# Kernel optimization log

Measured on AMD Instinct MI355X. Metric: run time of the kernel, lower is better.

Reference implementation:

```python
import jax, jax.numpy as jnp
import numpy as np

N, C, H = 4096, 1024, 16
HD = C // H            # 64
DR = HD // 8           # 8 rope freqs per spatial axis


def setup_inputs() -> dict:
    key = jax.random.key(0)
    k1, k2, k3, k4, k5, k6 = jax.random.split(key, 6)
    x = jax.random.normal(k1, (N, C), dtype=jnp.float32)
    coords = jax.random.randint(k2, (N, 5), 0, 64, dtype=jnp.int32)  # [batch, t, h, w, z]
    w_qkv = jax.random.normal(k3, (3 * C, C), dtype=jnp.float32) / np.sqrt(C)
    w_out = jax.random.normal(k4, (C, C), dtype=jnp.float32) / np.sqrt(C)
    gamma_q = jnp.ones((H, HD), dtype=jnp.float32)
    gamma_k = jnp.ones((H, HD), dtype=jnp.float32)
    return {"x": x, "coords": coords, "w_qkv": w_qkv, "w_out": w_out,
            "gamma_q": gamma_q, "gamma_k": gamma_k}


def _rms_norm(t, gamma):
    # F.normalize(dim=-1) * gamma * sqrt(head_dim), computed in fp32
    t = t.astype(jnp.float32)
    nrm = jnp.linalg.norm(t, axis=-1, keepdims=True)
    return t / jnp.maximum(nrm, 1e-12) * gamma * np.float32(np.sqrt(HD))


def _rope_angles(coords):
    # freqs = 1/10000^(arange(DR)/HD); angles per axis (t,h,w,z), concat -> [N, 4*DR] = [N, HD/2]
    freqs = 1.0 / (10000.0 ** (jnp.arange(DR, dtype=jnp.float32) / HD))
    pos = coords[:, 1:].astype(jnp.float32)  # [N,4]
    ang = pos[:, :, None] * freqs[None, None, :]  # [N,4,DR]
    return ang.reshape(ang.shape[0], -1)  # [N, HD/2]


def _apply_rope(t, cos, sin):
    # t: [N,H,HD]; pairs (2i, 2i+1) rotated by angle[i]
    t2 = t.astype(jnp.float32).reshape(t.shape[0], t.shape[1], -1, 2)
    re = t2[..., 0] * cos - t2[..., 1] * sin
    im = t2[..., 0] * sin + t2[..., 1] * cos
    return jnp.stack([re, im], axis=-1).reshape(t.shape)


def reference(x, coords, w_qkv, w_out, gamma_q, gamma_k):
    n = x.shape[0]
    qkv = (x @ w_qkv.T).reshape(n, 3, H, HD)
    q, k, v = qkv[:, 0], qkv[:, 1], qkv[:, 2]  # [N,H,HD]
    q = _rms_norm(q, gamma_q)
    k = _rms_norm(k, gamma_k)
    ang = _rope_angles(coords)              # [N, HD/2]
    cos = jnp.cos(ang)[:, None, :]          # [N,1,HD/2] (broadcast over heads)
    sin = jnp.sin(ang)[:, None, :]
    q = _apply_rope(q, cos, sin)
    k = _apply_rope(k, cos, sin)
    scale = np.float32(1.0 / np.sqrt(HD))
    scores = jnp.einsum('nhd,mhd->hnm', q, k) * scale  # [H,N,N]
    attn = jax.nn.softmax(scores, axis=-1)
    out = jnp.einsum('hnm,mhd->nhd', attn, v).reshape(n, C)
    return out @ w_out.T
```

## Files before the change

kernel.cpp:

```cpp
#include <hip/hip_runtime.h>
#include <hip/hip_bf16.h>

typedef _Float16 half8 __attribute__((ext_vector_type(8)));
typedef _Float16 half4v __attribute__((ext_vector_type(4)));
typedef _Float16 half2 __attribute__((ext_vector_type(2)));
typedef float f32x4 __attribute__((ext_vector_type(4)));

constexpr int NT = 4096;
constexpr int CH = 1024;
constexpr int NH = 16;
constexpr int HD = 64;
constexpr int C3 = 3072;

#if __has_builtin(__builtin_amdgcn_exp2f)
#define EXP2(x) __builtin_amdgcn_exp2f(x)
#else
#define EXP2(x) exp2f(x)
#endif

#define GLOAD_LDS16(gp, lp) __builtin_amdgcn_global_load_lds( \
    (const __attribute__((address_space(1))) void*)(gp),      \
    (__attribute__((address_space(3))) void*)(lp), 16, 0, 0)

static __device__ inline half2 pk_f16(float a, float b) {
  auto r = __builtin_amdgcn_cvt_pkrtz(a, b);
  return *(half2*)&r;
}

__global__ __launch_bounds__(256) void cvt_kernel(const float* __restrict__ in,
                                                  _Float16* __restrict__ out, int n4) {
  int i = blockIdx.x * 256 + threadIdx.x;
  if (i >= n4) return;
  float4 v = ((const float4*)in)[i];
  half4v h;
  h[0] = (_Float16)v.x; h[1] = (_Float16)v.y; h[2] = (_Float16)v.z; h[3] = (_Float16)v.w;
  ((half4v*)out)[i] = h;
}

template <typename OutT>
__global__ __launch_bounds__(256) void gemm_bt(const _Float16* __restrict__ A,
                                               const _Float16* __restrict__ Bt,
                                               OutT* __restrict__ Cc,
                                               int M, int Nn, int K) {
  __shared__ _Float16 As[128][32];
  __shared__ _Float16 Bs[128][32];
  const int tid = threadIdx.x;
  const int lane = tid & 63, w = tid >> 6;
  const int l15 = lane & 15, l4 = lane >> 4;
  const int m0 = blockIdx.x * 128, n0 = blockIdx.y * 128;
  const int wr = w >> 1, wc = w & 1;
  const int rb = w * 32;
  const int rl = lane >> 2;
  const int cb = (lane & 3) * 8;
  f32x4 acc[4][4] = {};
  for (int k0 = 0; k0 < K; k0 += 32) {
    __syncthreads();
    GLOAD_LDS16(A  + (size_t)(m0 + rb + rl) * K + k0 + cb,      &As[rb][0]);
    GLOAD_LDS16(A  + (size_t)(m0 + rb + 16 + rl) * K + k0 + cb, &As[rb + 16][0]);
    GLOAD_LDS16(Bt + (size_t)(n0 + rb + rl) * K + k0 + cb,      &Bs[rb][0]);
    GLOAD_LDS16(Bt + (size_t)(n0 + rb + 16 + rl) * K + k0 + cb, &Bs[rb + 16][0]);
    __syncthreads();
    half8 af[4], bf[4];
#pragma unroll
    for (int mt = 0; mt < 4; ++mt) af[mt] = *(half8*)&As[wr * 64 + mt * 16 + l15][l4 * 8];
#pragma unroll
    for (int nt = 0; nt < 4; ++nt) bf[nt] = *(half8*)&Bs[wc * 64 + nt * 16 + l15][l4 * 8];
#pragma unroll
    for (int mt = 0; mt < 4; ++mt)
#pragma unroll
      for (int nt = 0; nt < 4; ++nt)
        acc[mt][nt] = __builtin_amdgcn_mfma_f32_16x16x32_f16(af[mt], bf[nt], acc[mt][nt], 0, 0, 0);
  }
#pragma unroll
  for (int mt = 0; mt < 4; ++mt)
#pragma unroll
    for (int nt = 0; nt < 4; ++nt)
#pragma unroll
      for (int r = 0; r < 4; ++r) {
        int row = m0 + wr * 64 + mt * 16 + l4 * 4 + r;
        int col = n0 + wc * 64 + nt * 16 + l15;
        Cc[(size_t)row * Nn + col] = (OutT)acc[mt][nt][r];
      }
}

__global__ __launch_bounds__(256) void rmsrope_kernel(const _Float16* __restrict__ qkv,
                                                      const int* __restrict__ coords,
                                                      const float* __restrict__ gq,
                                                      const float* __restrict__ gk,
                                                      _Float16* __restrict__ Qh,
                                                      _Float16* __restrict__ Kh) {
  int gw = blockIdx.x * 4 + (threadIdx.x >> 6);
  int lane = threadIdx.x & 63;
  int n = gw >> 4, h = gw & 15;
  float q = (float)qkv[(size_t)n * C3 + h * HD + lane];
  float k = (float)qkv[(size_t)n * C3 + CH + h * HD + lane];
  float sq = q * q, sk = k * k;
#pragma unroll
  for (int m = 1; m < 64; m <<= 1) { sq += __shfl_xor(sq, m); sk += __shfl_xor(sk, m); }
  q *= 8.0f / fmaxf(sqrtf(sq), 1e-12f) * gq[h * HD + lane];
  k *= 8.0f / fmaxf(sqrtf(sk), 1e-12f) * gk[h * HD + lane];
  int j = lane >> 1, p = j >> 3, dr = j & 7;
  float ang = (float)coords[n * 5 + 1 + p] * __expf(-(float)dr * 0.14391157f);
  float cs = cosf(ang), sn = sinf(ang);
  float qp = __shfl_xor(q, 1), kp = __shfl_xor(k, 1);
  float qr, kr;
  if ((lane & 1) == 0) { qr = q * cs - qp * sn; kr = k * cs - kp * sn; }
  else                 { qr = qp * sn + q * cs; kr = kp * sn + k * cs; }
  size_t o = ((size_t)h * NT + n) * HD + lane;
  Qh[o] = (_Float16)(qr * 0.18033688f);
  Kh[o] = (_Float16)kr;
}

__global__ __launch_bounds__(256) void vtrans_kernel(const _Float16* __restrict__ qkv,
                                                     _Float16* __restrict__ VT) {
  __shared__ _Float16 L[64][72];
  int h = blockIdx.y, n0 = blockIdx.x * 64, t = threadIdx.x;
#pragma unroll
  for (int i = 0; i < 2; ++i) {
    int cid = t + i * 256, r = cid >> 3, c = cid & 7;
    *(half8*)&L[r][c * 8] = *(const half8*)(qkv + (size_t)(n0 + r) * C3 + 2 * CH + h * HD + c * 8);
  }
  __syncthreads();
#pragma unroll
  for (int i = 0; i < 2; ++i) {
    int cid = t + i * 256, d = cid >> 3, c = cid & 7;
    half8 v;
#pragma unroll
    for (int jj = 0; jj < 8; ++jj) v[jj] = L[c * 8 + jj][d];
    *(half8*)(VT + ((size_t)h * HD + d) * NT + n0 + c * 8) = v;
  }
}

__global__ __launch_bounds__(256, 2) void attn_kernel(const _Float16* __restrict__ Qh,
                                                      const _Float16* __restrict__ Kh,
                                                      const _Float16* __restrict__ VT,
                                                      _Float16* __restrict__ Oh) {
  __shared__ _Float16 Ks[64][72];
  __shared__ _Float16 Vs[64][72];
  const int tid = threadIdx.x, lane = tid & 63, w = tid >> 6;
  const int l15 = lane & 15, l4 = lane >> 4;
  int bid = blockIdx.x;
  int s = bid >> 3;
  int h = (bid & 7) * 2 + (s >> 5);
  int n0 = (s & 31) * 128;
  half8 qf[2][2];
#pragma unroll
  for (int qb = 0; qb < 2; ++qb)
#pragma unroll
    for (int kk = 0; kk < 2; ++kk)
      qf[qb][kk] = *(const half8*)(Qh + ((size_t)h * NT + n0 + w * 32 + qb * 16 + l15) * HD + kk * 32 + l4 * 8);
  f32x4 acc[2][4] = {};
  f32x4 acc5[2] = {};
  half8 of1 = {};
  if (l15 == 0) {
#pragma unroll
    for (int j = 0; j < 8; ++j) of1[j] = (_Float16)1.0f;
  }
  const int gr0 = tid >> 3, gr1 = gr0 + 32, c = tid & 7;
  auto rho = [](int g) {
    return (g & 32) | (((g >> 2) & 1) << 4) | (((g >> 3) & 3) << 2) | (g & 3);
  };
  const int pr0 = rho(gr0), pr1 = rho(gr1);
  const _Float16* Kb = Kh + (size_t)h * NT * HD;
  const _Float16* Vb = VT + (size_t)h * HD * NT;
  half8 kA0, kA1, vA0, vA1, kB0, kB1, vB0, vB1;
  auto loadset = [&](int k0, half8& ka, half8& kb, half8& va, half8& vb) {
    ka = *(const half8*)(Kb + (size_t)(k0 + gr0) * HD + c * 8);
    kb = *(const half8*)(Kb + (size_t)(k0 + gr1) * HD + c * 8);
    va = *(const half8*)(Vb + (size_t)gr0 * NT + k0 + c * 8);
    vb = *(const half8*)(Vb + (size_t)gr1 * NT + k0 + c * 8);
  };
  auto storeset = [&](half8 ka, half8 kb, half8 va, half8 vb) {
    *(half8*)&Ks[pr0][c * 8] = ka;
    *(half8*)&Ks[pr1][c * 8] = kb;
    *(half8*)&Vs[gr0][c * 8] = va;
    *(half8*)&Vs[gr1][c * 8] = vb;
  };
  auto compute = [&]() {
    f32x4 sv[2][4] = {};
    __builtin_amdgcn_s_setprio(1);
#pragma unroll
    for (int t = 0; t < 4; ++t) {
      half8 kf0 = *(half8*)&Ks[t * 16 + l15][l4 * 8];
      half8 kf1 = *(half8*)&Ks[t * 16 + l15][32 + l4 * 8];
      sv[0][t] = __builtin_amdgcn_mfma_f32_16x16x32_f16(kf0, qf[0][0], sv[0][t], 0, 0, 0);
      sv[0][t] = __builtin_amdgcn_mfma_f32_16x16x32_f16(kf1, qf[0][1], sv[0][t], 0, 0, 0);
      sv[1][t] = __builtin_amdgcn_mfma_f32_16x16x32_f16(kf0, qf[1][0], sv[1][t], 0, 0, 0);
      sv[1][t] = __builtin_amdgcn_mfma_f32_16x16x32_f16(kf1, qf[1][1], sv[1][t], 0, 0, 0);
    }
    __builtin_amdgcn_s_setprio(0);
    union U { half8 v; half2 p[4]; };
    U u[2][2];
#pragma unroll
    for (int qb = 0; qb < 2; ++qb) {
      float e[4][4];
#pragma unroll
      for (int t = 0; t < 4; ++t)
#pragma unroll
        for (int r = 0; r < 4; ++r) e[t][r] = EXP2(sv[qb][t][r]);
      u[qb][0].p[0] = pk_f16(e[0][0], e[0][1]); u[qb][0].p[1] = pk_f16(e[0][2], e[0][3]);
      u[qb][0].p[2] = pk_f16(e[1][0], e[1][1]); u[qb][0].p[3] = pk_f16(e[1][2], e[1][3]);
      u[qb][1].p[0] = pk_f16(e[2][0], e[2][1]); u[qb][1].p[1] = pk_f16(e[2][2], e[2][3]);
      u[qb][1].p[2] = pk_f16(e[3][0], e[3][1]); u[qb][1].p[3] = pk_f16(e[3][2], e[3][3]);
    }
    __builtin_amdgcn_s_setprio(1);
#pragma unroll
    for (int t = 0; t < 4; ++t) {
      half8 vf0 = *(half8*)&Vs[t * 16 + l15][l4 * 8];
      half8 vf1 = *(half8*)&Vs[t * 16 + l15][32 + l4 * 8];
      acc[0][t] = __builtin_amdgcn_mfma_f32_16x16x32_f16(u[0][0].v, vf0, acc[0][t], 0, 0, 0);
      acc[0][t] = __builtin_amdgcn_mfma_f32_16x16x32_f16(u[0][1].v, vf1, acc[0][t], 0, 0, 0);
      acc[1][t] = __builtin_amdgcn_mfma_f32_16x16x32_f16(u[1][0].v, vf0, acc[1][t], 0, 0, 0);
      acc[1][t] = __builtin_amdgcn_mfma_f32_16x16x32_f16(u[1][1].v, vf1, acc[1][t], 0, 0, 0);
    }
    acc5[0] = __builtin_amdgcn_mfma_f32_16x16x32_f16(u[0][0].v, of1, acc5[0], 0, 0, 0);
    acc5[0] = __builtin_amdgcn_mfma_f32_16x16x32_f16(u[0][1].v, of1, acc5[0], 0, 0, 0);
    acc5[1] = __builtin_amdgcn_mfma_f32_16x16x32_f16(u[1][0].v, of1, acc5[1], 0, 0, 0);
    acc5[1] = __builtin_amdgcn_mfma_f32_16x16x32_f16(u[1][1].v, of1, acc5[1], 0, 0, 0);
    __builtin_amdgcn_s_setprio(0);
  };
  loadset(0, kA0, kA1, vA0, vA1);
  for (int k0 = 0; k0 < NT; k0 += 128) {
    __syncthreads();
    storeset(kA0, kA1, vA0, vA1);
    __syncthreads();
    loadset(k0 + 64, kB0, kB1, vB0, vB1);
    compute();
    __syncthreads();
    storeset(kB0, kB1, vB0, vB1);
    __syncthreads();
    if (k0 + 128 < NT) loadset(k0 + 128, kA0, kA1, vA0, vA1);
    compute();
  }
#pragma unroll
  for (int qb = 0; qb < 2; ++qb) {
    float linv[4];
#pragma unroll
    for (int r = 0; r < 4; ++r) linv[r] = 1.0f / __shfl(acc5[qb][r], lane & 48);
#pragma unroll
    for (int t = 0; t < 4; ++t)
#pragma unroll
      for (int r = 0; r < 4; ++r) {
        int row = n0 + w * 32 + qb * 16 + l4 * 4 + r;
        Oh[(size_t)row * CH + h * HD + t * 16 + l15] = (_Float16)(acc[qb][t][r] * linv[r]);
      }
  }
}

extern "C" void kernel_launch(void* const* d_in, const int* in_sizes, int n_in,
                              void* d_out, int out_size, void* d_ws, size_t ws_size,
                              hipStream_t stream) {
  const float* x      = (const float*)d_in[0];
  const int*   coords = (const int*)d_in[1];
  const float* w_qkv  = (const float*)d_in[2];
  const float* w_out  = (const float*)d_in[3];
  const float* gq     = (const float*)d_in[4];
  const float* gk     = (const float*)d_in[5];
  float* out = (float*)d_out;

  char* ws = (char*)d_ws;
  size_t off = 0;
  auto alloc = [&](size_t bytes) { char* p = ws + off; off += bytes; return p; };
  _Float16* xh   = (_Float16*)alloc((size_t)NT * CH * 2);
  _Float16* wqh  = (_Float16*)alloc((size_t)C3 * CH * 2);
  _Float16* woh  = (_Float16*)alloc((size_t)CH * CH * 2);
  _Float16* qkvh = (_Float16*)alloc((size_t)NT * C3 * 2);
  _Float16* Qh   = (_Float16*)alloc((size_t)NT * CH * 2);
  _Float16* Kh   = (_Float16*)alloc((size_t)NT * CH * 2);
  _Float16* VTh  = (_Float16*)alloc((size_t)NT * CH * 2);
  _Float16* Oh   = (_Float16*)alloc((size_t)NT * CH * 2);
  if (off > ws_size) return;

  cvt_kernel<<<NT * CH / 4 / 256, 256, 0, stream>>>(x, xh, NT * CH / 4);
  cvt_kernel<<<C3 * CH / 4 / 256, 256, 0, stream>>>(w_qkv, wqh, C3 * CH / 4);
  cvt_kernel<<<CH * CH / 4 / 256, 256, 0, stream>>>(w_out, woh, CH * CH / 4);
  gemm_bt<_Float16><<<dim3(NT / 128, C3 / 128), 256, 0, stream>>>(xh, wqh, qkvh, NT, C3, CH);
  rmsrope_kernel<<<NT * NH / 4, 256, 0, stream>>>(qkvh, coords, gq, gk, Qh, Kh);
  vtrans_kernel<<<dim3(NT / 64, NH), 256, 0, stream>>>(qkvh, VTh);
  attn_kernel<<<NH * (NT / 128), 256, 0, stream>>>(Qh, Kh, VTh, Oh);
  gemm_bt<float><<<dim3(NT / 128, CH / 128), 256, 0, stream>>>(Oh, woh, out, NT, CH, CH);
}
```

Measured before the change: 176.0 us.

## Pre-swizzle K and V into MFMA fragment order and drop LDS staging in attention

The rmsrope and V-transpose kernels now write K and V in a layout that matches the per-lane MFMA operand order for each 64-key block. The attention kernel then loads fragments straight from global memory into registers with coalesced 16-byte loads, with no shared-memory tiles and no block barriers. The aim is to remove the LDS round trip and the four __syncthreads per 128 keys. In exchange, every wave reloads the full K/V tile from global memory or L2 instead of sharing it through LDS, and the double-buffered register sets raise register pressure.

```diff
diff --git a/kernel.cpp b/kernel.cpp
--- a/kernel.cpp
+++ b/kernel.cpp
@@ -88,7 +88,7 @@
                                                       const float* __restrict__ gq,
                                                       const float* __restrict__ gk,
                                                       _Float16* __restrict__ Qh,
-                                                      _Float16* __restrict__ Kh) {
+                                                      _Float16* __restrict__ KF) {
   int gw = blockIdx.x * 4 + (threadIdx.x >> 6);
   int lane = threadIdx.x & 63;
   int n = gw >> 4, h = gw & 15;
@@ -106,37 +106,41 @@
   float qr, kr;
   if ((lane & 1) == 0) { qr = q * cs - qp * sn; kr = k * cs - kp * sn; }
   else                 { qr = qp * sn + q * cs; kr = kp * sn + k * cs; }
-  size_t o = ((size_t)h * NT + n) * HD + lane;
-  Qh[o] = (_Float16)(qr * 0.18033688f);
-  Kh[o] = (_Float16)kr;
+  Qh[((size_t)h * NT + n) * HD + lane] = (_Float16)(qr * 0.18033688f);
+  int m64 = n & 63, kb = n >> 6;
+  int t   = 2 * (m64 >> 5) + ((m64 >> 2) & 1);
+  int i15 = 4 * ((m64 >> 3) & 3) + (m64 & 3);
+  int kk = lane >> 5, ll4 = (lane >> 3) & 3, jj = lane & 7;
+  KF[(size_t)h * NT * HD + (size_t)kb * 4096 +
+     (size_t)(((t * 2 + kk) * 64 + ll4 * 16 + i15) * 8 + jj)] = (_Float16)kr;
 }
 
 __global__ __launch_bounds__(256) void vtrans_kernel(const _Float16* __restrict__ qkv,
-                                                     _Float16* __restrict__ VT) {
+                                                     _Float16* __restrict__ VF) {
   __shared__ _Float16 L[64][72];
-  int h = blockIdx.y, n0 = blockIdx.x * 64, t = threadIdx.x;
+  int h = blockIdx.y, n0 = blockIdx.x * 64, kb = blockIdx.x, t0 = threadIdx.x;
 #pragma unroll
   for (int i = 0; i < 2; ++i) {
-    int cid = t + i * 256, r = cid >> 3, c = cid & 7;
+    int cid = t0 + i * 256, r = cid >> 3, c = cid & 7;
     *(half8*)&L[r][c * 8] = *(const half8*)(qkv + (size_t)(n0 + r) * C3 + 2 * CH + h * HD + c * 8);
   }
   __syncthreads();
 #pragma unroll
   for (int i = 0; i < 2; ++i) {
-    int cid = t + i * 256, d = cid >> 3, c = cid & 7;
+    int cid = t0 + i * 256, d = cid >> 3, c = cid & 7;
     half8 v;
 #pragma unroll
     for (int jj = 0; jj < 8; ++jj) v[jj] = L[c * 8 + jj][d];
-    *(half8*)(VT + ((size_t)h * HD + d) * NT + n0 + c * 8) = v;
+    size_t flat = (size_t)h * NT * HD + (size_t)kb * 4096 +
+                  (size_t)((((d >> 4) * 2 + (c >> 2)) * 64 + (c & 3) * 16 + (d & 15)) * 8);
+    *(half8*)(VF + flat) = v;
   }
 }
 
 __global__ __launch_bounds__(256, 2) void attn_kernel(const _Float16* __restrict__ Qh,
-                                                      const _Float16* __restrict__ Kh,
-                                                      const _Float16* __restrict__ VT,
+                                                      const _Float16* __restrict__ KF,
+                                                      const _Float16* __restrict__ VF,
                                                       _Float16* __restrict__ Oh) {
-  __shared__ _Float16 Ks[64][72];
-  __shared__ _Float16 Vs[64][72];
   const int tid = threadIdx.x, lane = tid & 63, w = tid >> 6;
   const int l15 = lane & 15, l4 = lane >> 4;
   int bid = blockIdx.x;
@@ -154,40 +158,30 @@
   half8 of1 = {};
   if (l15 == 0) {
 #pragma unroll
-    for (int j = 0; j < 8; ++j) of1[j] = (_Float16)1.0f;
-  }
-  const int gr0 = tid >> 3, gr1 = gr0 + 32, c = tid & 7;
-  auto rho = [](int g) {
-    return (g & 32) | (((g >> 2) & 1) << 4) | (((g >> 3) & 3) << 2) | (g & 3);
+    for (int jq = 0; jq < 8; ++jq) of1[jq] = (_Float16)1.0f;
+  }
+  const _Float16* KFb = KF + (size_t)h * NT * HD + lane * 8;
+  const _Float16* VFb = VF + (size_t)h * NT * HD + lane * 8;
+  half8 kA[8], vA[8], kB[8], vB[8];
+  auto loadset = [&](int kb, half8 (&k)[8], half8 (&v)[8]) {
+    const _Float16* kp = KFb + (size_t)kb * 4096;
+    const _Float16* vp = VFb + (size_t)kb * 4096;
+#pragma unroll
+    for (int f = 0; f < 8; ++f) {
+      k[f] = *(const half8*)(kp + f * 512);
+      v[f] = *(const half8*)(vp + f * 512);
+    }
   };
-  const int pr0 = rho(gr0), pr1 = rho(gr1);
-  const _Float16* Kb = Kh + (size_t)h * NT * HD;
-  const _Float16* Vb = VT + (size_t)h * HD * NT;
-  half8 kA0, kA1, vA0, vA1, kB0, kB1, vB0, vB1;
-  auto loadset = [&](int k0, half8& ka, half8& kb, half8& va, half8& vb) {
-    ka = *(const half8*)(Kb + (size_t)(k0 + gr0) * HD + c * 8);
-    kb = *(const half8*)(Kb + (size_t)(k0 + gr1) * HD + c * 8);
-    va = *(const half8*)(Vb + (size_t)gr0 * NT + k0 + c * 8);
-    vb = *(const half8*)(Vb + (size_t)gr1 * NT + k0 + c * 8);
-  };
-  auto storeset = [&](half8 ka, half8 kb, half8 va, half8 vb) {
-    *(half8*)&Ks[pr0][c * 8] = ka;
-    *(half8*)&Ks[pr1][c * 8] = kb;
-    *(half8*)&Vs[gr0][c * 8] = va;
-    *(half8*)&Vs[gr1][c * 8] = vb;
-  };
-  auto compute = [&]() {
+  auto compute = [&](half8 (&k)[8], half8 (&v)[8]) {
     f32x4 sv[2][4] = {};
     __builtin_amdgcn_s_setprio(1);
 #pragma unroll
-    for (int t = 0; t < 4; ++t) {
-      half8 kf0 = *(half8*)&Ks[t * 16 + l15][l4 * 8];
-      half8 kf1 = *(half8*)&Ks[t * 16 + l15][32 + l4 * 8];
-      sv[0][t] = __builtin_amdgcn_mfma_f32_16x16x32_f16(kf0, qf[0][0], sv[0][t], 0, 0, 0);
-      sv[0][t] = __builtin_amdgcn_mfma_f32_16x16x32_f16(kf1, qf[0][1], sv[0][t], 0, 0, 0);
-      sv[1][t] = __builtin_amdgcn_mfma_f32_16x16x32_f16(kf0, qf[1][0], sv[1][t], 0, 0, 0);
-      sv[1][t] = __builtin_amdgcn_mfma_f32_16x16x32_f16(kf1, qf[1][1], sv[1][t], 0, 0, 0);
-    }
+    for (int t = 0; t < 4; ++t)
+#pragma unroll
+      for (int kk = 0; kk < 2; ++kk) {
+        sv[0][t] = __builtin_amdgcn_mfma_f32_16x16x32_f16(k[t * 2 + kk], qf[0][kk], sv[0][t], 0, 0, 0);
+        sv[1][t] = __builtin_amdgcn_mfma_f32_16x16x32_f16(k[t * 2 + kk], qf[1][kk], sv[1][t], 0, 0, 0);
+      }
     __builtin_amdgcn_s_setprio(0);
     union U { half8 v; half2 p[4]; };
     U u[2][2];
@@ -205,32 +199,24 @@
     }
     __builtin_amdgcn_s_setprio(1);
 #pragma unroll
-    for (int t = 0; t < 4; ++t) {
-      half8 vf0 = *(half8*)&Vs[t * 16 + l15][l4 * 8];
-      half8 vf1 = *(half8*)&Vs[t * 16 + l15][32 + l4 * 8];
-      acc[0][t] = __builtin_amdgcn_mfma_f32_16x16x32_f16(u[0][0].v, vf0, acc[0][t], 0, 0, 0);
-      acc[0][t] = __builtin_amdgcn_mfma_f32_16x16x32_f16(u[0][1].v, vf1, acc[0][t], 0, 0, 0);
-      acc[1][t] = __builtin_amdgcn_mfma_f32_16x16x32_f16(u[1][0].v, vf0, acc[1][t], 0, 0, 0);
-      acc[1][t] = __builtin_amdgcn_mfma_f32_16x16x32_f16(u[1][1].v, vf1, acc[1][t], 0, 0, 0);
-    }
+    for (int t = 0; t < 4; ++t)
+#pragma unroll
+      for (int kk = 0; kk < 2; ++kk) {
+        acc[0][t] = __builtin_amdgcn_mfma_f32_16x16x32_f16(u[0][kk].v, v[t * 2 + kk], acc[0][t], 0, 0, 0);
+        acc[1][t] = __builtin_amdgcn_mfma_f32_16x16x32_f16(u[1][kk].v, v[t * 2 + kk], acc[1][t], 0, 0, 0);
+      }
     acc5[0] = __builtin_amdgcn_mfma_f32_16x16x32_f16(u[0][0].v, of1, acc5[0], 0, 0, 0);
     acc5[0] = __builtin_amdgcn_mfma_f32_16x16x32_f16(u[0][1].v, of1, acc5[0], 0, 0, 0);
     acc5[1] = __builtin_amdgcn_mfma_f32_16x16x32_f16(u[1][0].v, of1, acc5[1], 0, 0, 0);
     acc5[1] = __builtin_amdgcn_mfma_f32_16x16x32_f16(u[1][1].v, of1, acc5[1], 0, 0, 0);
     __builtin_amdgcn_s_setprio(0);
   };
-  loadset(0, kA0, kA1, vA0, vA1);
-  for (int k0 = 0; k0 < NT; k0 += 128) {
-    __syncthreads();
-    storeset(kA0, kA1, vA0, vA1);
-    __syncthreads();
-    loadset(k0 + 64, kB0, kB1, vB0, vB1);
-    compute();
-    __syncthreads();
-    storeset(kB0, kB1, vB0, vB1);
-    __syncthreads();
-    if (k0 + 128 < NT) loadset(k0 + 128, kA0, kA1, vA0, vA1);
-    compute();
+  loadset(0, kA, vA);
+  for (int kb = 0; kb < 64; kb += 2) {
+    loadset(kb + 1, kB, vB);
+    compute(kA, vA);
+    if (kb + 2 < 64) loadset(kb + 2, kA, vA);
+    compute(kB, vB);
   }
 #pragma unroll
   for (int qb = 0; qb < 2; ++qb) {
@@ -266,8 +252,8 @@
   _Float16* woh  = (_Float16*)alloc((size_t)CH * CH * 2);
   _Float16* qkvh = (_Float16*)alloc((size_t)NT * C3 * 2);
   _Float16* Qh   = (_Float16*)alloc((size_t)NT * CH * 2);
-  _Float16* Kh   = (_Float16*)alloc((size_t)NT * CH * 2);
-  _Float16* VTh  = (_Float16*)alloc((size_t)NT * CH * 2);
+  _Float16* KFh  = (_Float16*)alloc((size_t)NT * CH * 2);
+  _Float16* VFh  = (_Float16*)alloc((size_t)NT * CH * 2);
   _Float16* Oh   = (_Float16*)alloc((size_t)NT * CH * 2);
   if (off > ws_size) return;
 
@@ -275,8 +261,8 @@
   cvt_kernel<<<C3 * CH / 4 / 256, 256, 0, stream>>>(w_qkv, wqh, C3 * CH / 4);
   cvt_kernel<<<CH * CH / 4 / 256, 256, 0, stream>>>(w_out, woh, CH * CH / 4);
   gemm_bt<_Float16><<<dim3(NT / 128, C3 / 128), 256, 0, stream>>>(xh, wqh, qkvh, NT, C3, CH);
-  rmsrope_kernel<<<NT * NH / 4, 256, 0, stream>>>(qkvh, coords, gq, gk, Qh, Kh);
-  vtrans_kernel<<<dim3(NT / 64, NH), 256, 0, stream>>>(qkvh, VTh);
-  attn_kernel<<<NH * (NT / 128), 256, 0, stream>>>(Qh, Kh, VTh, Oh);
+  rmsrope_kernel<<<NT * NH / 4, 256, 0, stream>>>(qkvh, coords, gq, gk, Qh, KFh);
+  vtrans_kernel<<<dim3(NT / 64, NH), 256, 0, stream>>>(qkvh, VFh);
+  attn_kernel<<<NH * (NT / 128), 256, 0, stream>>>(Qh, KFh, VFh, Oh);
   gemm_bt<float><<<dim3(NT / 128, CH / 128), 256, 0, stream>>>(Oh, woh, out, NT, CH, CH);
 }
```

New measurement: 186.2 us. +5.7%, slower.
